# Optimization experiments

Measured on AMD Instinct MI355X. Metric: run time of the kernel, lower is better.

## Reference

```python
import jax, jax.numpy as jnp
import numpy as np

NHEAD = 16


def setup_inputs() -> dict:
    key = jax.random.key(0)
    ks = jax.random.split(key, 6)
    S, B, D = 2048, 2, 1024
    std = float(np.sqrt(6.0 / (D + D)))  # xavier_uniform bound
    inp = {
        "query": jax.random.normal(ks[0], (S, B, D), jnp.float32),
        "key": jax.random.normal(ks[1], (S, B, D), jnp.float32),
        "value": jax.random.normal(ks[2], (S, B, D), jnp.float32),
        "Wq": jax.random.uniform(ks[3], (D, D), jnp.float32, -std, std),
        "bq": jnp.ones((D,), jnp.float32),
        "Wk": jax.random.uniform(ks[4], (D, D), jnp.float32, -std, std),
        "bk": jnp.ones((D,), jnp.float32),
        "Wv": jax.random.uniform(ks[5], (D, D), jnp.float32, -std, std),
        "bv": jnp.ones((D,), jnp.float32),
    }
    return inp


def reference(query, key, value, Wq, bq, Wk, bk, Wv, bv):
    S, B, D = query.shape
    h = NHEAD
    d = D // h
    scale = jnp.asarray(d ** 0.5, query.dtype)
    # projections (nn.Linear: x @ W^T + b)
    q = (query @ Wq.T + bq).reshape(S, B, h, d)
    k = (key @ Wk.T + bk).reshape(S, B, h, d)
    v = (value @ Wv.T + bv).reshape(S, B, h, d)
    # batch_first=False path: scores [b,h,i,j], softmax over j, then AV
    scores = jnp.einsum('ibhd,jbhd->bhij', q, k) / scale
    attn = jax.nn.softmax(scores, axis=-1)
    out = jnp.einsum('bhij,jbhd->ibhd', attn, v).reshape(S, B, D)
    return out
```

## Files before the change

kernel.cpp:

```cpp
#include <hip/hip_runtime.h>
#include <hip/hip_bf16.h>

#define S_LEN 2048
#define BATCH 2
#define DMODEL 1024
#define NHEAD 16
#define HDIM 64
#define MTOT (S_LEN * BATCH)
#define QKV_ELEMS ((size_t)MTOT * DMODEL)

typedef __bf16 bf16x8 __attribute__((ext_vector_type(8)));
typedef unsigned short u16x8 __attribute__((ext_vector_type(8)));
typedef float f32x4 __attribute__((ext_vector_type(4)));
typedef float f32x16 __attribute__((ext_vector_type(16)));
typedef unsigned int u32x4 __attribute__((ext_vector_type(4)));

__device__ __forceinline__ unsigned short f2bf(float f) {
    unsigned int u = __float_as_uint(f);
    u += 0x7FFFu + ((u >> 16) & 1u);
    return (unsigned short)(u >> 16);
}

__device__ __forceinline__ void gload_lds16(const void* g, void* l) {
    __builtin_amdgcn_global_load_lds(
        (const __attribute__((address_space(1))) unsigned int*)g,
        (__attribute__((address_space(3))) unsigned int*)l, 16, 0, 0);
}

#define PBM 128
#define PBN 128
#define PBK 32
#define PLDS 48
#define QSCALE 0.18033688011112042f

__global__ __launch_bounds__(256) void proj_kernel(
        const float* __restrict__ Xq, const float* __restrict__ Xk,
        const float* __restrict__ Xv, const float* __restrict__ Wq,
        const float* __restrict__ Wk, const float* __restrict__ Wv,
        const float* __restrict__ bq, const float* __restrict__ bk,
        const float* __restrict__ bv, unsigned short* __restrict__ ws)
{
    const int t = blockIdx.z;
    const float* X    = (t == 0) ? Xq : (t == 1) ? Xk : Xv;
    const float* W    = (t == 0) ? Wq : (t == 1) ? Wk : Wv;
    const float* bias = (t == 0) ? bq : (t == 1) ? bk : bv;
    unsigned short* out = ws + (size_t)t * QKV_ELEMS;
    const float scale = (t == 0) ? QSCALE : 1.0f;

    __shared__ __align__(16) unsigned short lds[(PBM + PBN) * PLDS];
    unsigned short* Alds = lds;
    unsigned short* Blds = lds + PBM * PLDS;

    const int tid = threadIdx.x;
    const int m0 = blockIdx.y * PBM;
    const int n0 = blockIdx.x * PBN;

    const int wave = tid >> 6;
    const int lane = tid & 63;
    const int lrow = lane & 15;
    const int lg   = lane >> 4;
    const int wr = (wave >> 1) * 64;
    const int wc = (wave & 1) * 64;

    f32x4 acc[4][4];
#pragma unroll
    for (int i = 0; i < 4; ++i)
#pragma unroll
        for (int j = 0; j < 4; ++j)
            acc[i][j] = (f32x4){0.f, 0.f, 0.f, 0.f};

    const int sr = tid >> 3;
    const int sg = tid & 7;

    for (int k0 = 0; k0 < DMODEL; k0 += PBK) {
        __syncthreads();
#pragma unroll
        for (int it = 0; it < 4; ++it) {
            const int row = sr + it * 32;
            const float4 va = *(const float4*)(X + (size_t)(m0 + row) * DMODEL + k0 + sg * 4);
            const float4 vb = *(const float4*)(W + (size_t)(n0 + row) * DMODEL + k0 + sg * 4);
            ushort4 ha, hb;
            ha.x = f2bf(va.x); ha.y = f2bf(va.y); ha.z = f2bf(va.z); ha.w = f2bf(va.w);
            hb.x = f2bf(vb.x); hb.y = f2bf(vb.y); hb.z = f2bf(vb.z); hb.w = f2bf(vb.w);
            *(ushort4*)&Alds[row * PLDS + sg * 4] = ha;
            *(ushort4*)&Blds[row * PLDS + sg * 4] = hb;
        }
        __syncthreads();

        bf16x8 af[4], bw[4];
#pragma unroll
        for (int i = 0; i < 4; ++i) {
            af[i] = *(const bf16x8*)&Alds[(wr + i * 16 + lrow) * PLDS + lg * 8];
            bw[i] = *(const bf16x8*)&Blds[(wc + i * 16 + lrow) * PLDS + lg * 8];
        }
#pragma unroll
        for (int i = 0; i < 4; ++i)
#pragma unroll
            for (int j = 0; j < 4; ++j)
                acc[i][j] = __builtin_amdgcn_mfma_f32_16x16x32_bf16(af[i], bw[j], acc[i][j], 0, 0, 0);
    }

#pragma unroll
    for (int j = 0; j < 4; ++j) {
        const int n  = n0 + wc + j * 16 + lrow;
        const float bv_ = bias[n];
        const int h  = n >> 6;
        const int dd = n & 63;
#pragma unroll
        for (int i = 0; i < 4; ++i) {
#pragma unroll
            for (int r = 0; r < 4; ++r) {
                const int m = m0 + wr + i * 16 + lg * 4 + r;
                const int s = m >> 1;
                const int b = m & 1;
                const float v = (acc[i][j][r] + bv_) * scale;
                size_t idx;
                if (t == 2)
                    idx = ((size_t)((b * NHEAD + h) * HDIM + dd)) * S_LEN + s;
                else
                    idx = ((size_t)((b * NHEAD + h) * S_LEN + s)) * HDIM + dd;
                out[idx] = f2bf(v);
            }
        }
    }
}

#define NT (S_LEN / 64)

__global__ __launch_bounds__(256) void attn_kernel(
        const unsigned short* __restrict__ ws, float* __restrict__ out)
{
    const unsigned short* Qw = ws;
    const unsigned short* Kw = ws + QKV_ELEMS;
    const unsigned short* Vw = ws + 2 * QKV_ELEMS;

    const int bid = blockIdx.x;
    const int idx = bid >> 3;
    const int bh  = (bid & 7) * 4 + (idx >> 4);
    const int q0  = (idx & 15) * 128;

    __shared__ __align__(16) unsigned short Kbuf[2][64 * 64];
    __shared__ __align__(16) unsigned short Vbuf[2][64 * 64];
    __shared__ unsigned int Pu[4][32 * 32];

    const int tid  = threadIdx.x;
    const int wave = tid >> 6;
    const int lane = tid & 63;
    const int l31  = lane & 31;
    const int half = lane >> 5;

    const size_t base = (size_t)bh * S_LEN * HDIM;
    const int qrow = q0 + wave * 32 + l31;

    bf16x8 qf[4];
#pragma unroll
    for (int c = 0; c < 4; ++c)
        qf[c] = *(const bf16x8*)(Qw + base + (size_t)qrow * HDIM + c * 16 + half * 8);

    f32x16 Od0, Od1;
#pragma unroll
    for (int i = 0; i < 16; ++i) { Od0[i] = 0.f; Od1[i] = 0.f; }
    float mrun = -__builtin_inff();
    float lrun = 0.f;

    const int strow = lane >> 3;
    const int sgrp  = (lane & 7) ^ strow;
    const int r0    = wave * 16 + strow;
    const int dstoff = wave * 1024 + lane * 8;

    gload_lds16(Kw + base + (size_t)r0 * HDIM + sgrp * 8,        &Kbuf[0][dstoff]);
    gload_lds16(Kw + base + (size_t)(r0 + 8) * HDIM + sgrp * 8,  &Kbuf[0][dstoff + 512]);
    gload_lds16(Vw + base + (size_t)r0 * S_LEN + sgrp * 8,       &Vbuf[0][dstoff]);
    gload_lds16(Vw + base + (size_t)(r0 + 8) * S_LEN + sgrp * 8, &Vbuf[0][dstoff + 512]);
    __syncthreads();

    int cur = 0;
    for (int t = 0; t < NT; ++t) {
        if (t + 1 < NT) {
            const int sn = (t + 1) * 64;
            gload_lds16(Kw + base + (size_t)(sn + r0) * HDIM + sgrp * 8,       &Kbuf[cur ^ 1][dstoff]);
            gload_lds16(Kw + base + (size_t)(sn + r0 + 8) * HDIM + sgrp * 8,   &Kbuf[cur ^ 1][dstoff + 512]);
            gload_lds16(Vw + base + (size_t)r0 * S_LEN + sn + sgrp * 8,        &Vbuf[cur ^ 1][dstoff]);
            gload_lds16(Vw + base + (size_t)(r0 + 8) * S_LEN + sn + sgrp * 8,  &Vbuf[cur ^ 1][dstoff + 512]);
        }

        const unsigned short* Klds = Kbuf[cur];
        const unsigned short* Vlds = Vbuf[cur];

        f32x16 S0, S1;
#pragma unroll
        for (int i = 0; i < 16; ++i) { S0[i] = 0.f; S1[i] = 0.f; }
        __builtin_amdgcn_s_setprio(1);
#pragma unroll
        for (int c = 0; c < 4; ++c) {
            const int g = ((c * 2 + half) ^ (l31 & 7)) * 8;
            const bf16x8 ka0 = *(const bf16x8*)&Klds[l31 * 64 + g];
            const bf16x8 ka1 = *(const bf16x8*)&Klds[(32 + l31) * 64 + g];
            S0 = __builtin_amdgcn_mfma_f32_32x32x16_bf16(ka0, qf[c], S0, 0, 0, 0);
            S1 = __builtin_amdgcn_mfma_f32_32x32x16_bf16(ka1, qf[c], S1, 0, 0, 0);
        }
        __builtin_amdgcn_s_setprio(0);

        f32x16 mx16;
#pragma unroll
        for (int i = 0; i < 16; ++i) mx16[i] = fmaxf(S0[i], S1[i]);
        float m8[8], m4[4], m2[2];
#pragma unroll
        for (int i = 0; i < 8; ++i) m8[i] = fmaxf(mx16[i], mx16[i + 8]);
#pragma unroll
        for (int i = 0; i < 4; ++i) m4[i] = fmaxf(m8[i], m8[i + 4]);
        m2[0] = fmaxf(m4[0], m4[2]); m2[1] = fmaxf(m4[1], m4[3]);
        float mx = fmaxf(m2[0], m2[1]);
        mx = fmaxf(mx, __shfl_xor(mx, 32, 64));

        if (!__all(mx - mrun <= 8.0f)) {
            const float mnew = fmaxf(mrun, mx);
            const float ex   = exp2f(mrun - mnew);
            mrun = mnew;
            lrun *= ex;
            Od0 *= ex;
            Od1 *= ex;
        }

#pragma unroll
        for (int i = 0; i < 16; ++i) S0[i] = exp2f(S0[i] - mrun);
#pragma unroll
        for (int i = 0; i < 16; ++i) S1[i] = exp2f(S1[i] - mrun);
        f32x16 sv = S0 + S1;
        float s8[8], s4[4];
#pragma unroll
        for (int i = 0; i < 8; ++i) s8[i] = sv[i] + sv[i + 8];
#pragma unroll
        for (int i = 0; i < 4; ++i) s4[i] = s8[i] + s8[i + 4];
        float psum = (s4[0] + s4[2]) + (s4[1] + s4[3]);
        psum += __shfl_xor(psum, 32, 64);
        lrun += psum;

#pragma unroll
        for (int w = 0; w < 8; ++w) {
            const unsigned int pk0 = (unsigned int)f2bf(S0[2 * w])
                                   | ((unsigned int)f2bf(S0[2 * w + 1]) << 16);
            const unsigned int pk1 = (unsigned int)f2bf(S1[2 * w])
                                   | ((unsigned int)f2bf(S1[2 * w + 1]) << 16);
            const int kp = (w & 1) + 4 * (w >> 1) + 2 * half;
            Pu[wave][kp * 32 + l31]        = pk0;
            Pu[wave][(16 + kp) * 32 + l31] = pk1;
        }
        __asm__ volatile("" ::: "memory");

        __builtin_amdgcn_s_setprio(1);
#pragma unroll
        for (int c = 0; c < 4; ++c) {
            const int g = ((c * 2 + half) ^ (l31 & 7)) * 8;
            const bf16x8 va0 = *(const bf16x8*)&Vlds[l31 * 64 + g];
            const bf16x8 va1 = *(const bf16x8*)&Vlds[(32 + l31) * 64 + g];
            u32x4 pu;
#pragma unroll
            for (int e = 0; e < 4; ++e)
                pu[e] = Pu[wave][(c * 8 + half * 4 + e) * 32 + l31];
            const bf16x8 pb = __builtin_bit_cast(bf16x8, pu);
            Od0 = __builtin_amdgcn_mfma_f32_32x32x16_bf16(va0, pb, Od0, 0, 0, 0);
            Od1 = __builtin_amdgcn_mfma_f32_32x32x16_bf16(va1, pb, Od1, 0, 0, 0);
        }
        __builtin_amdgcn_s_setprio(0);

        __syncthreads();
        cur ^= 1;
    }

    const int bb = bh >> 4;
    const int hh = bh & 15;
    const float inv = 1.0f / lrun;
    float* op = out + (size_t)qrow * (BATCH * DMODEL) + bb * DMODEL + hh * HDIM;
#pragma unroll
    for (int gg = 0; gg < 4; ++gg) {
        const int d0 = gg * 8 + half * 4;
        float4 v0, v1;
        v0.x = Od0[gg * 4 + 0] * inv; v0.y = Od0[gg * 4 + 1] * inv;
        v0.z = Od0[gg * 4 + 2] * inv; v0.w = Od0[gg * 4 + 3] * inv;
        v1.x = Od1[gg * 4 + 0] * inv; v1.y = Od1[gg * 4 + 1] * inv;
        v1.z = Od1[gg * 4 + 2] * inv; v1.w = Od1[gg * 4 + 3] * inv;
        *(float4*)(op + d0)      = v0;
        *(float4*)(op + 32 + d0) = v1;
    }
}

extern "C" void kernel_launch(void* const* d_in, const int* in_sizes, int n_in,
                              void* d_out, int out_size, void* d_ws, size_t ws_size,
                              hipStream_t stream) {
    const float* q  = (const float*)d_in[0];
    const float* k  = (const float*)d_in[1];
    const float* v  = (const float*)d_in[2];
    const float* Wq = (const float*)d_in[3];
    const float* bq = (const float*)d_in[4];
    const float* Wk = (const float*)d_in[5];
    const float* bk = (const float*)d_in[6];
    const float* Wv = (const float*)d_in[7];
    const float* bv = (const float*)d_in[8];
    unsigned short* ws = (unsigned short*)d_ws;
    float* out = (float*)d_out;

    dim3 pgrid(DMODEL / PBN, MTOT / PBM, 3);
    proj_kernel<<<pgrid, dim3(256), 0, stream>>>(q, k, v, Wq, Wk, Wv, bq, bk, bv, ws);

    attn_kernel<<<dim3(512), dim3(256), 0, stream>>>(ws, out);
}
```

Before: 160.9 us.

## Prefetch projection tiles into registers and widen attention blocks to 8 waves

The projection GEMM now loads the next K-slice of X and W into registers while the current slice is being multiplied, so global load latency overlaps the MFMA work. Attention blocks grow from 4 to 8 waves (256 query rows each) with half as many blocks, so each K/V tile staged in LDS serves twice as many query rows and the per-thread staging loads drop from four to two. The cost is more register pressure in the projection and only 256 attention blocks, which may leave some CUs underused.

```diff
diff --git a/kernel.cpp b/kernel.cpp
--- a/kernel.cpp
+++ b/kernel.cpp
@@ -72,20 +72,36 @@
     const int sr = tid >> 3;
     const int sg = tid & 7;
 
+    float4 a_r[4], b_r[4];
+#pragma unroll
+    for (int it = 0; it < 4; ++it) {
+        const int row = sr + it * 32;
+        a_r[it] = *(const float4*)(X + (size_t)(m0 + row) * DMODEL + sg * 4);
+        b_r[it] = *(const float4*)(W + (size_t)(n0 + row) * DMODEL + sg * 4);
+    }
+
     for (int k0 = 0; k0 < DMODEL; k0 += PBK) {
-        __syncthreads();
 #pragma unroll
         for (int it = 0; it < 4; ++it) {
             const int row = sr + it * 32;
-            const float4 va = *(const float4*)(X + (size_t)(m0 + row) * DMODEL + k0 + sg * 4);
-            const float4 vb = *(const float4*)(W + (size_t)(n0 + row) * DMODEL + k0 + sg * 4);
             ushort4 ha, hb;
-            ha.x = f2bf(va.x); ha.y = f2bf(va.y); ha.z = f2bf(va.z); ha.w = f2bf(va.w);
-            hb.x = f2bf(vb.x); hb.y = f2bf(vb.y); hb.z = f2bf(vb.z); hb.w = f2bf(vb.w);
+            ha.x = f2bf(a_r[it].x); ha.y = f2bf(a_r[it].y);
+            ha.z = f2bf(a_r[it].z); ha.w = f2bf(a_r[it].w);
+            hb.x = f2bf(b_r[it].x); hb.y = f2bf(b_r[it].y);
+            hb.z = f2bf(b_r[it].z); hb.w = f2bf(b_r[it].w);
             *(ushort4*)&Alds[row * PLDS + sg * 4] = ha;
             *(ushort4*)&Blds[row * PLDS + sg * 4] = hb;
         }
         __syncthreads();
+
+        if (k0 + PBK < DMODEL) {
+#pragma unroll
+            for (int it = 0; it < 4; ++it) {
+                const int row = sr + it * 32;
+                a_r[it] = *(const float4*)(X + (size_t)(m0 + row) * DMODEL + k0 + PBK + sg * 4);
+                b_r[it] = *(const float4*)(W + (size_t)(n0 + row) * DMODEL + k0 + PBK + sg * 4);
+            }
+        }
 
         bf16x8 af[4], bw[4];
 #pragma unroll
@@ -98,6 +114,8 @@
 #pragma unroll
             for (int j = 0; j < 4; ++j)
                 acc[i][j] = __builtin_amdgcn_mfma_f32_16x16x32_bf16(af[i], bw[j], acc[i][j], 0, 0, 0);
+
+        __syncthreads();
     }
 
 #pragma unroll
@@ -127,7 +145,7 @@
 
 #define NT (S_LEN / 64)
 
-__global__ __launch_bounds__(256) void attn_kernel(
+__global__ __launch_bounds__(512) void attn_kernel(
         const unsigned short* __restrict__ ws, float* __restrict__ out)
 {
     const unsigned short* Qw = ws;
@@ -136,12 +154,12 @@
 
     const int bid = blockIdx.x;
     const int idx = bid >> 3;
-    const int bh  = (bid & 7) * 4 + (idx >> 4);
-    const int q0  = (idx & 15) * 128;
+    const int bh  = (bid & 7) * 4 + (idx >> 3);
+    const int q0  = (idx & 7) * 256;
 
     __shared__ __align__(16) unsigned short Kbuf[2][64 * 64];
     __shared__ __align__(16) unsigned short Vbuf[2][64 * 64];
-    __shared__ unsigned int Pu[4][32 * 32];
+    __shared__ unsigned int Pu[8][32 * 32];
 
     const int tid  = threadIdx.x;
     const int wave = tid >> 6;
@@ -163,25 +181,20 @@
     float mrun = -__builtin_inff();
     float lrun = 0.f;
 
-    const int strow = lane >> 3;
-    const int sgrp  = (lane & 7) ^ strow;
-    const int r0    = wave * 16 + strow;
-    const int dstoff = wave * 1024 + lane * 8;
-
-    gload_lds16(Kw + base + (size_t)r0 * HDIM + sgrp * 8,        &Kbuf[0][dstoff]);
-    gload_lds16(Kw + base + (size_t)(r0 + 8) * HDIM + sgrp * 8,  &Kbuf[0][dstoff + 512]);
-    gload_lds16(Vw + base + (size_t)r0 * S_LEN + sgrp * 8,       &Vbuf[0][dstoff]);
-    gload_lds16(Vw + base + (size_t)(r0 + 8) * S_LEN + sgrp * 8, &Vbuf[0][dstoff + 512]);
+    const int srow = tid >> 3;
+    const int sgrp = (tid & 7) ^ (srow & 7);
+    const int dsto = tid * 8;
+
+    gload_lds16(Kw + base + (size_t)srow * HDIM + sgrp * 8,  &Kbuf[0][dsto]);
+    gload_lds16(Vw + base + (size_t)srow * S_LEN + sgrp * 8, &Vbuf[0][dsto]);
     __syncthreads();
 
     int cur = 0;
     for (int t = 0; t < NT; ++t) {
         if (t + 1 < NT) {
             const int sn = (t + 1) * 64;
-            gload_lds16(Kw + base + (size_t)(sn + r0) * HDIM + sgrp * 8,       &Kbuf[cur ^ 1][dstoff]);
-            gload_lds16(Kw + base + (size_t)(sn + r0 + 8) * HDIM + sgrp * 8,   &Kbuf[cur ^ 1][dstoff + 512]);
-            gload_lds16(Vw + base + (size_t)r0 * S_LEN + sn + sgrp * 8,        &Vbuf[cur ^ 1][dstoff]);
-            gload_lds16(Vw + base + (size_t)(r0 + 8) * S_LEN + sn + sgrp * 8,  &Vbuf[cur ^ 1][dstoff + 512]);
+            gload_lds16(Kw + base + (size_t)(sn + srow) * HDIM + sgrp * 8, &Kbuf[cur ^ 1][dsto]);
+            gload_lds16(Vw + base + (size_t)srow * S_LEN + sn + sgrp * 8, &Vbuf[cur ^ 1][dsto]);
         }
 
         const unsigned short* Klds = Kbuf[cur];
@@ -303,5 +316,5 @@
     dim3 pgrid(DMODEL / PBN, MTOT / PBM, 3);
     proj_kernel<<<pgrid, dim3(256), 0, stream>>>(q, k, v, Wq, Wk, Wv, bq, bk, bv, ws);
 
-    attn_kernel<<<dim3(512), dim3(256), 0, stream>>>(ws, out);
-}
+    attn_kernel<<<dim3(256), dim3(512), 0, stream>>>(ws, out);
+}
```

Result: slower. 172.0 us (+6.9%).
